# Optimization experiments

Measured on AMD Instinct MI355X. Metric: run time of the kernel, lower is better.

## Reference

```python
import jax, jax.numpy as jnp
import numpy as np

N = 10000
E = 320000
F_IN = 512
NHID = 32
LATENT = 16


def setup_inputs() -> dict:
    key = jax.random.key(0)
    k1, k2, k3, k4, k5 = jax.random.split(key, 5)
    x = jax.random.normal(k1, (N, F_IN), dtype=jnp.float32)
    W1 = jax.random.normal(k2, (F_IN, NHID), dtype=jnp.float32) * (1.0 / np.sqrt(F_IN))
    W2 = jax.random.normal(k3, (NHID, LATENT), dtype=jnp.float32) * (1.0 / np.sqrt(NHID))
    edge_index = jax.random.randint(k4, (2, E), 0, N, dtype=jnp.int32)
    edge_weight = jax.random.uniform(k5, (E,), dtype=jnp.float32)
    return {"x": x, "W1": W1, "W2": W2, "edge_index": edge_index,
            "edge_weight": edge_weight}


def _spmm(edge_index, edge_weight, h):
    # out[dst] += w * h[src]  (sparse normalized-adjacency matmul)
    src, dst = edge_index[0], edge_index[1]
    msgs = edge_weight[:, None] * h[src]          # [E, D] gather + scale
    return jax.ops.segment_sum(msgs, dst, num_segments=N)  # [N, D]


def reference(x, W1, W2, edge_index, edge_weight):
    # GCNConv layer 1: adj @ (x @ W1)
    h = _spmm(edge_index, edge_weight, x @ W1)    # [N, NHID]
    # GCNConv layer 2: adj @ (h @ W2)
    z = _spmm(edge_index, edge_weight, h @ W2)    # [N, LATENT]
    # Inner-product decoder: sigmoid(z @ z^T)
    adj_recon = jax.nn.sigmoid(z @ z.T)           # [N, N]
    return adj_recon, z
```

## Files before the change

kernel.cpp:

```cpp
#include <hip/hip_runtime.h>
#include <cstdint>
#include <cstddef>

#define N_NODES 10000
#define F_IN    512
#define NHID    32
#define LATENT  16

typedef float v4f __attribute__((ext_vector_type(4)));

__global__ __launch_bounds__(256) void gemm1_kernel(const float* __restrict__ x,
                                                    const float* __restrict__ W1,
                                                    float* __restrict__ h0,
                                                    float* __restrict__ h,
                                                    float* __restrict__ z) {
    const int gid = blockIdx.x * 256 + threadIdx.x;
    h[gid] = 0.f;
    if (gid < N_NODES * LATENT) z[gid] = 0.f;

    __shared__ float xs[8][F_IN];
    const int row0 = blockIdx.x * 8;
    for (int t = threadIdx.x; t < 8 * F_IN; t += 256) {
        const int r = t >> 9;
        const int c = t & (F_IN - 1);
        xs[r][c] = x[(size_t)(row0 + r) * F_IN + c];
    }
    __syncthreads();

    const int col = threadIdx.x & 31;
    const int r   = threadIdx.x >> 5;
    float a0 = 0.f, a1 = 0.f, a2 = 0.f, a3 = 0.f;
#pragma unroll 4
    for (int k = 0; k < F_IN; k += 4) {
        const float4 xv = *(const float4*)&xs[r][k];
        a0 += xv.x * W1[(k + 0) * NHID + col];
        a1 += xv.y * W1[(k + 1) * NHID + col];
        a2 += xv.z * W1[(k + 2) * NHID + col];
        a3 += xv.w * W1[(k + 3) * NHID + col];
    }
    h0[(size_t)(row0 + r) * NHID + col] = (a0 + a1) + (a2 + a3);
}

template <int D>
__global__ __launch_bounds__(256) void spmm_kernel(const int* __restrict__ src,
                                                   const int* __restrict__ dst,
                                                   const float* __restrict__ w,
                                                   const float* __restrict__ hin,
                                                   float* __restrict__ hout,
                                                   int E) {
    const int idx = blockIdx.x * 256 + threadIdx.x;
    const int e = idx / D;
    const int d = idx & (D - 1);
    if (e < E) {
        const int s = src[e];
        const int t = dst[e];
        const float val = w[e] * hin[(size_t)s * D + d];
        atomicAdd(&hout[(size_t)t * D + d], val);
    }
}

__global__ __launch_bounds__(256) void gemm2_kernel(const float* __restrict__ h,
                                                    const float* __restrict__ W2,
                                                    float* __restrict__ z0) {
    __shared__ float w2s[NHID * LATENT];
    for (int t = threadIdx.x; t < NHID * LATENT; t += 256) w2s[t] = W2[t];
    __syncthreads();

    const int idx = blockIdx.x * 256 + threadIdx.x;
    if (idx < N_NODES * LATENT) {
        const int row = idx >> 4;
        const int col = idx & (LATENT - 1);
        const float* __restrict__ hr = h + (size_t)row * NHID;
        float acc = 0.f;
#pragma unroll
        for (int k = 0; k < NHID; ++k) acc += hr[k] * w2s[k * LATENT + col];
        z0[idx] = acc;
    }
}

#define TI 32

__device__ __forceinline__ float sigmoid_fast(float x) {
    return __builtin_amdgcn_rcpf(1.0f + __expf(-x));
}

__global__ __launch_bounds__(256) void decoder_kernel(const float* __restrict__ z,
                                                      float* __restrict__ out) {
    const int j0 = (blockIdx.x * 256 + threadIdx.x) << 2;
    const int i0 = blockIdx.y * TI;
    if (j0 >= N_NODES) return;

    float4 zj0[4], zj1[4], zj2[4], zj3[4];
    {
        const float4* zp0 = (const float4*)(z + (size_t)(j0 + 0) * LATENT);
        const float4* zp1 = (const float4*)(z + (size_t)(j0 + 1) * LATENT);
        const float4* zp2 = (const float4*)(z + (size_t)(j0 + 2) * LATENT);
        const float4* zp3 = (const float4*)(z + (size_t)(j0 + 3) * LATENT);
#pragma unroll
        for (int p = 0; p < 4; ++p) {
            zj0[p] = zp0[p]; zj1[p] = zp1[p]; zj2[p] = zp2[p]; zj3[p] = zp3[p];
        }
    }

    const int imax = min(TI, N_NODES - i0);
#pragma unroll 2
    for (int ii = 0; ii < imax; ++ii) {
        const float4* __restrict__ zi = (const float4*)(z + (size_t)(i0 + ii) * LATENT);
        const float4 a0 = zi[0], a1 = zi[1], a2 = zi[2], a3 = zi[3];

        v4f r;
        r.x = a0.x*zj0[0].x + a0.y*zj0[0].y + a0.z*zj0[0].z + a0.w*zj0[0].w
            + a1.x*zj0[1].x + a1.y*zj0[1].y + a1.z*zj0[1].z + a1.w*zj0[1].w
            + a2.x*zj0[2].x + a2.y*zj0[2].y + a2.z*zj0[2].z + a2.w*zj0[2].w
            + a3.x*zj0[3].x + a3.y*zj0[3].y + a3.z*zj0[3].z + a3.w*zj0[3].w;
        r.y = a0.x*zj1[0].x + a0.y*zj1[0].y + a0.z*zj1[0].z + a0.w*zj1[0].w
            + a1.x*zj1[1].x + a1.y*zj1[1].y + a1.z*zj1[1].z + a1.w*zj1[1].w
            + a2.x*zj1[2].x + a2.y*zj1[2].y + a2.z*zj1[2].z + a2.w*zj1[2].w
            + a3.x*zj1[3].x + a3.y*zj1[3].y + a3.z*zj1[3].z + a3.w*zj1[3].w;
        r.z = a0.x*zj2[0].x + a0.y*zj2[0].y + a0.z*zj2[0].z + a0.w*zj2[0].w
            + a1.x*zj2[1].x + a1.y*zj2[1].y + a1.z*zj2[1].z + a1.w*zj2[1].w
            + a2.x*zj2[2].x + a2.y*zj2[2].y + a2.z*zj2[2].z + a2.w*zj2[2].w
            + a3.x*zj2[3].x + a3.y*zj2[3].y + a3.z*zj2[3].z + a3.w*zj2[3].w;
        r.w = a0.x*zj3[0].x + a0.y*zj3[0].y + a0.z*zj3[0].z + a0.w*zj3[0].w
            + a1.x*zj3[1].x + a1.y*zj3[1].y + a1.z*zj3[1].z + a1.w*zj3[1].w
            + a2.x*zj3[2].x + a2.y*zj3[2].y + a2.z*zj3[2].z + a2.w*zj3[2].w
            + a3.x*zj3[3].x + a3.y*zj3[3].y + a3.z*zj3[3].z + a3.w*zj3[3].w;

        r.x = sigmoid_fast(r.x);
        r.y = sigmoid_fast(r.y);
        r.z = sigmoid_fast(r.z);
        r.w = sigmoid_fast(r.w);

        __builtin_nontemporal_store(
            r, (v4f*)(out + (size_t)(i0 + ii) * N_NODES + j0));
    }
}

extern "C" void kernel_launch(void* const* d_in, const int* in_sizes, int n_in,
                              void* d_out, int out_size, void* d_ws, size_t ws_size,
                              hipStream_t stream) {
    const float* x  = (const float*)d_in[0];
    const float* W1 = (const float*)d_in[1];
    const float* W2 = (const float*)d_in[2];
    const int*   ei = (const int*)d_in[3];
    const float* ew = (const float*)d_in[4];
    const int E = in_sizes[3] / 2;
    const int* src = ei;
    const int* dst = ei + E;

    float* out = (float*)d_out;
    float* z   = out + (size_t)N_NODES * N_NODES;

    float* h0 = out;
    float* h  = h0 + N_NODES * NHID;
    float* z0 = h  + N_NODES * NHID;

    gemm1_kernel<<<N_NODES / 8, 256, 0, stream>>>(x, W1, h0, h, z);
    spmm_kernel<NHID><<<(E * NHID + 255) / 256, 256, 0, stream>>>(src, dst, ew, h0, h, E);

    gemm2_kernel<<<(N_NODES * LATENT + 255) / 256, 256, 0, stream>>>(h, W2, z0);
    spmm_kernel<LATENT><<<(E * LATENT + 255) / 256, 256, 0, stream>>>(src, dst, ew, z0, z, E);

    dim3 dgrid((N_NODES / 4 + 255) / 256, (N_NODES + TI - 1) / TI);
    decoder_kernel<<<dgrid, 256, 0, stream>>>(z, out);
}
```

Measured before the change: 502.7 us.

## Precompute W1@W2 and reassociate so both SpMMs run at width 16

Since there is no nonlinearity between the layers, the model is linear: A(A X W1)W2 = A A (X (W1 W2)). The change precomputes W12 = W1·W2 in a small kernel, projects x straight to 16 columns, and runs both sparse aggregations at width 16 instead of 32 and 16. The separate gemm2 kernel is removed. This halves the atomic scatter traffic of the first SpMM at the cost of one tiny extra launch and a change in floating-point summation order.

Measured after the change: 479.3 us. -4.7%, faster.

```diff
diff --git a/kernel.cpp b/kernel.cpp
--- a/kernel.cpp
+++ b/kernel.cpp
@@ -9,36 +9,53 @@
 
 typedef float v4f __attribute__((ext_vector_type(4)));
 
+
+__global__ __launch_bounds__(256) void w12_kernel(const float* __restrict__ W1,
+                                                  const float* __restrict__ W2,
+                                                  float* __restrict__ W12) {
+    __shared__ float w2s[NHID * LATENT];
+    for (int t = threadIdx.x; t < NHID * LATENT; t += 256) w2s[t] = W2[t];
+    __syncthreads();
+
+    const int idx = blockIdx.x * 256 + threadIdx.x;
+    const int r = idx >> 4;
+    const int c = idx & (LATENT - 1);
+    float acc = 0.f;
+#pragma unroll
+    for (int k = 0; k < NHID; ++k) acc += W1[r * NHID + k] * w2s[k * LATENT + c];
+    W12[idx] = acc;
+}
+
 __global__ __launch_bounds__(256) void gemm1_kernel(const float* __restrict__ x,
-                                                    const float* __restrict__ W1,
-                                                    float* __restrict__ h0,
-                                                    float* __restrict__ h,
+                                                    const float* __restrict__ W12,
+                                                    float* __restrict__ g0,
+                                                    float* __restrict__ g1,
                                                     float* __restrict__ z) {
     const int gid = blockIdx.x * 256 + threadIdx.x;
-    h[gid] = 0.f;
-    if (gid < N_NODES * LATENT) z[gid] = 0.f;
+    g1[gid] = 0.f;
+    z[gid]  = 0.f;
 
-    __shared__ float xs[8][F_IN];
-    const int row0 = blockIdx.x * 8;
-    for (int t = threadIdx.x; t < 8 * F_IN; t += 256) {
+    __shared__ float xs[16][F_IN];
+    const int row0 = blockIdx.x * 16;
+    for (int t = threadIdx.x; t < 16 * F_IN; t += 256) {
         const int r = t >> 9;
         const int c = t & (F_IN - 1);
         xs[r][c] = x[(size_t)(row0 + r) * F_IN + c];
     }
     __syncthreads();
 
-    const int col = threadIdx.x & 31;
-    const int r   = threadIdx.x >> 5;
+    const int col = threadIdx.x & 15;
+    const int r   = threadIdx.x >> 4;
     float a0 = 0.f, a1 = 0.f, a2 = 0.f, a3 = 0.f;
 #pragma unroll 4
     for (int k = 0; k < F_IN; k += 4) {
         const float4 xv = *(const float4*)&xs[r][k];
-        a0 += xv.x * W1[(k + 0) * NHID + col];
-        a1 += xv.y * W1[(k + 1) * NHID + col];
-        a2 += xv.z * W1[(k + 2) * NHID + col];
-        a3 += xv.w * W1[(k + 3) * NHID + col];
+        a0 += xv.x * W12[(k + 0) * LATENT + col];
+        a1 += xv.y * W12[(k + 1) * LATENT + col];
+        a2 += xv.z * W12[(k + 2) * LATENT + col];
+        a3 += xv.w * W12[(k + 3) * LATENT + col];
     }
-    h0[(size_t)(row0 + r) * NHID + col] = (a0 + a1) + (a2 + a3);
+    g0[(size_t)(row0 + r) * LATENT + col] = (a0 + a1) + (a2 + a3);
 }
 
 template <int D>
@@ -56,25 +73,6 @@
         const int t = dst[e];
         const float val = w[e] * hin[(size_t)s * D + d];
         atomicAdd(&hout[(size_t)t * D + d], val);
-    }
-}
-
-__global__ __launch_bounds__(256) void gemm2_kernel(const float* __restrict__ h,
-                                                    const float* __restrict__ W2,
-                                                    float* __restrict__ z0) {
-    __shared__ float w2s[NHID * LATENT];
-    for (int t = threadIdx.x; t < NHID * LATENT; t += 256) w2s[t] = W2[t];
-    __syncthreads();
-
-    const int idx = blockIdx.x * 256 + threadIdx.x;
-    if (idx < N_NODES * LATENT) {
-        const int row = idx >> 4;
-        const int col = idx & (LATENT - 1);
-        const float* __restrict__ hr = h + (size_t)row * NHID;
-        float acc = 0.f;
-#pragma unroll
-        for (int k = 0; k < NHID; ++k) acc += hr[k] * w2s[k * LATENT + col];
-        z0[idx] = acc;
     }
 }
 
@@ -151,15 +149,16 @@
     float* out = (float*)d_out;
     float* z   = out + (size_t)N_NODES * N_NODES;
 
-    float* h0 = out;
-    float* h  = h0 + N_NODES * NHID;
-    float* z0 = h  + N_NODES * NHID;
+    float* g0  = out;
+    float* g1  = g0 + N_NODES * LATENT;
+    float* W12 = g1 + N_NODES * LATENT;
 
-    gemm1_kernel<<<N_NODES / 8, 256, 0, stream>>>(x, W1, h0, h, z);
-    spmm_kernel<NHID><<<(E * NHID + 255) / 256, 256, 0, stream>>>(src, dst, ew, h0, h, E);
+    w12_kernel<<<(F_IN * LATENT) / 256, 256, 0, stream>>>(W1, W2, W12);
 
-    gemm2_kernel<<<(N_NODES * LATENT + 255) / 256, 256, 0, stream>>>(h, W2, z0);
-    spmm_kernel<LATENT><<<(E * LATENT + 255) / 256, 256, 0, stream>>>(src, dst, ew, z0, z, E);
+    gemm1_kernel<<<N_NODES / 16, 256, 0, stream>>>(x, W12, g0, g1, z);
+
+    spmm_kernel<LATENT><<<(E * LATENT + 255) / 256, 256, 0, stream>>>(src, dst, ew, g0, g1, E);
+    spmm_kernel<LATENT><<<(E * LATENT + 255) / 256, 256, 0, stream>>>(src, dst, ew, g1, z, E);
 
     dim3 dgrid((N_NODES / 4 + 255) / 256, (N_NODES + TI - 1) / TI);
     decoder_kernel<<<dgrid, 256, 0, stream>>>(z, out);
```
